# Optimization experiments

Hardware: AMD Instinct MI355X
Metric: run time of the kernel (lower is better)

The kernel has to match this reference:

```python
import jax, jax.numpy as jnp
import numpy as np

H = 1024      # hidden_size
NH = 16       # num_heads
HD = H // NH  # head_dim


def setup_inputs() -> dict:
    key = jax.random.key(0)
    ks = jax.random.split(key, 12)
    inp = {
        "query": jax.random.normal(ks[0], (4, 1024, H), dtype=jnp.float32),
        "key": jax.random.normal(ks[1], (4, 2048, H), dtype=jnp.float32),
        "value": jax.random.normal(ks[2], (4, 2048, H), dtype=jnp.float32),
        "key_padding_mask": jax.random.randint(ks[3], (4, 2048), 0, 2, dtype=jnp.int32),
        # learned parameters (torch Linear: y = x @ W.T + b); we store W already transposed
        "Wq": jax.random.normal(ks[4], (H, H), dtype=jnp.float32) * (1.0 / np.sqrt(H)),
        "bq": jnp.zeros((H,), dtype=jnp.float32),
        "Wk": jax.random.normal(ks[5], (H, H), dtype=jnp.float32) * (1.0 / np.sqrt(H)),
        "bk": jnp.zeros((H,), dtype=jnp.float32),
        "Wv": jax.random.normal(ks[6], (H, H), dtype=jnp.float32) * (1.0 / np.sqrt(H)),
        "bv": jnp.zeros((H,), dtype=jnp.float32),
        "Wo": jax.random.normal(ks[7], (H, H), dtype=jnp.float32) * (1.0 / np.sqrt(H)),
        "bo": jnp.zeros((H,), dtype=jnp.float32),
    }
    return inp


def reference(query, key, value, key_padding_mask, Wq, bq, Wk, bk, Wv, bv, Wo, bo):
    B, Sq, _ = query.shape
    Sk = key.shape[1]
    scaling = HD ** -0.5
    # projections -> [B, NH, S, HD]
    q = (query @ Wq + bq).reshape(B, Sq, NH, HD).transpose(0, 2, 1, 3)
    k = (key @ Wk + bk).reshape(B, Sk, NH, HD).transpose(0, 2, 1, 3)
    v = (value @ Wv + bv).reshape(B, Sk, NH, HD).transpose(0, 2, 1, 3)
    # scores [B, NH, Sq, Sk]
    scores = jnp.einsum("bhqd,bhkd->bhqk", q, k) * scaling
    # mask: positions where key_padding_mask == 0 are ignored
    scores = jnp.where((key_padding_mask == 0)[:, None, None, :], -jnp.inf, scores)
    attn = jax.nn.softmax(scores, axis=-1)
    # dropout is identity in eval mode
    out = jnp.einsum("bhqk,bhkd->bhqd", attn, v)
    out = out.transpose(0, 2, 1, 3).reshape(B, Sq, H)
    return out @ Wo + bo
```

## Files before the change

kernel.cpp:

```cpp
#include <hip/hip_runtime.h>
#include <hip/hip_fp16.h>
#include <math.h>

#define B_ 4
#define SQ 1024
#define SK 2048
#define HH 1024
#define NHEAD 16
#define HDIM 64

typedef _Float16 f16;
typedef __attribute__((ext_vector_type(8))) _Float16 f16x8;
typedef __attribute__((ext_vector_type(4))) _Float16 f16x4;
typedef __attribute__((ext_vector_type(4))) float f32x4;
typedef unsigned int u32;
typedef unsigned long long u64;

#define GLOAD_LDS16(gp, lp) __builtin_amdgcn_global_load_lds( \
    (const __attribute__((address_space(1))) u32*)(gp),        \
    (__attribute__((address_space(3))) u32*)(lp), 16, 0, 0)

__global__ __launch_bounds__(256) void prep_k(
    const float* __restrict__ q, const float* __restrict__ k,
    const float* __restrict__ v,
    const float* __restrict__ W0, const float* __restrict__ W1,
    const float* __restrict__ W2, const float* __restrict__ W3,
    const int* __restrict__ mask,
    f16* __restrict__ qo, f16* __restrict__ ko, f16* __restrict__ vo,
    f16* __restrict__ WT, u32* __restrict__ pmask)
{
    __shared__ f16 t[64 * 80];
    const int bid = blockIdx.x, tid = threadIdx.x;
    if (bid < 10240) {
        int i = bid * 256 + tid;
        const float* src; f16* dst; int j;
        if (i < 524288)       { src = q; dst = qo; j = i; }
        else if (i < 1572864) { src = k; dst = ko; j = i - 524288; }
        else                  { src = v; dst = vo; j = i - 1572864; }
        float4 a = ((const float4*)src)[(size_t)j * 2];
        float4 b = ((const float4*)src)[(size_t)j * 2 + 1];
        f16x8 o;
        o[0] = (f16)a.x; o[1] = (f16)a.y; o[2] = (f16)a.z; o[3] = (f16)a.w;
        o[4] = (f16)b.x; o[5] = (f16)b.y; o[6] = (f16)b.z; o[7] = (f16)b.w;
        *(f16x8*)(dst + (size_t)j * 8) = o;
    } else if (bid < 11264) {
        int id = bid - 10240;
        int z = id >> 8, idx = id & 255;
        const float* W = z == 0 ? W0 : z == 1 ? W1 : z == 2 ? W2 : W3;
        f16* out = WT + (size_t)z * HH * HH;
        const int r0 = (idx >> 4) * 64, c0 = (idx & 15) * 64;
#pragma unroll
        for (int p = 0; p < 4; p++) {
            int s = p * 256 + tid;
            int row = s >> 4, u = s & 15;
            float4 a = *(const float4*)(W + (size_t)(r0 + row) * HH + c0 + u * 4);
            f16x4 vv;
            vv[0] = (f16)a.x; vv[1] = (f16)a.y; vv[2] = (f16)a.z; vv[3] = (f16)a.w;
            *(f16x4*)(t + row * 80 + u * 4) = vv;
        }
        __syncthreads();
#pragma unroll
        for (int p = 0; p < 2; p++) {
            int s = p * 256 + tid;
            int n = s >> 3, u = s & 7;
            f16x8 vv;
#pragma unroll
            for (int j = 0; j < 8; j++) vv[j] = t[(u * 8 + j) * 80 + n];
            *(f16x8*)(out + (size_t)(c0 + n) * HH + r0 + u * 8) = vv;
        }
    } else {
        int j = (bid - 11264) * 256 + tid;
        u64 bal = __ballot(mask[j] != 0);
        if ((tid & 63) == 0) *(u64*)(pmask + ((j >> 6) << 1)) = bal;
    }
}

template <int OUTMODE>
__global__ __launch_bounds__(256) void gemm_k(
    const f16* __restrict__ A, const f16* __restrict__ BT,
    const float* __restrict__ bias, void* __restrict__ Cout,
    int M, int K)
{
    __shared__ f16 sA[2][4096];
    __shared__ f16 sB[2][4096];
    const int tid = threadIdx.x, lane = tid & 63, w = tid >> 6;
    const int nwg = gridDim.x;
    const int swz = ((int)blockIdx.x & 7) * (nwg >> 3) + ((int)blockIdx.x >> 3);
    const int m0 = (swz >> 3) * 128;
    const int n0 = (swz & 7) * 128;
    const int wr = w >> 1, wc = w & 1;
    const int ql = lane & 15, g = lane >> 4;
    const int N = 1024;
    f32x4 acc[4][4] = {};

    auto stage = [&](int buf, int k0) {
#pragma unroll
        for (int p = 0; p < 2; p++) {
            int s = p * 256 + tid;
            int row = s >> 2, us = ((s & 3) ^ (row & 3)) * 8;
            f16* dst = &sA[buf][(p * 256 + w * 64) * 8];
            f16* dstB = &sB[buf][(p * 256 + w * 64) * 8];
            GLOAD_LDS16(A  + (size_t)(m0 + row) * K + k0 + us, dst);
            GLOAD_LDS16(BT + (size_t)(n0 + row) * K + k0 + us, dstB);
        }
    };

    stage(0, 0);
    int cur = 0;
    for (int k0 = 0; k0 < K; k0 += 32) {
        __syncthreads();
        if (k0 + 32 < K) stage(cur ^ 1, k0 + 32);
        f16x8 af[4], bf[4];
#pragma unroll
        for (int m = 0; m < 4; m++) {
            int row = wr * 64 + m * 16 + ql;
            af[m] = *(const f16x8*)(&sA[cur][row * 32 + ((g ^ (row & 3)) * 8)]);
        }
#pragma unroll
        for (int n = 0; n < 4; n++) {
            int row = wc * 64 + n * 16 + ql;
            bf[n] = *(const f16x8*)(&sB[cur][row * 32 + ((g ^ (row & 3)) * 8)]);
        }
#pragma unroll
        for (int m = 0; m < 4; m++)
#pragma unroll
            for (int n = 0; n < 4; n++)
                acc[m][n] = __builtin_amdgcn_mfma_f32_16x16x32_f16(af[m], bf[n], acc[m][n], 0, 0, 0);
        cur ^= 1;
    }

    float bv[4];
#pragma unroll
    for (int n = 0; n < 4; n++) bv[n] = bias[n0 + wc * 64 + n * 16 + ql];
#pragma unroll
    for (int m = 0; m < 4; m++) {
        int row0 = m0 + wr * 64 + m * 16 + g * 4;
#pragma unroll
        for (int n = 0; n < 4; n++) {
            int col = n0 + wc * 64 + n * 16 + ql;
            if (OUTMODE == 2) {
                int bb = row0 >> 11, kk = row0 & 2047;
                int hh = col >> 6, dd = col & 63;
                f16x4 vv;
#pragma unroll
                for (int e = 0; e < 4; e++) vv[e] = (f16)(acc[m][n][e] + bv[n]);
                *(f16x4*)((f16*)Cout + ((size_t)(bb * NHEAD + hh) * HDIM + dd) * SK + kk) = vv;
            } else if (OUTMODE == 1) {
#pragma unroll
                for (int e = 0; e < 4; e++)
                    ((f16*)Cout)[(size_t)(row0 + e) * N + col] = (f16)(acc[m][n][e] + bv[n]);
            } else {
#pragma unroll
                for (int e = 0; e < 4; e++)
                    ((float*)Cout)[(size_t)(row0 + e) * N + col] = acc[m][n][e] + bv[n];
            }
        }
    }
}

#define SC2 0.18033688f
#define THR2 11.5f

__global__ __launch_bounds__(512, 6) void attn_mfma_k(
    const f16* __restrict__ qp,
    const f16* __restrict__ kp,
    const f16* __restrict__ vt,
    const u32* __restrict__ pmask,
    f16* __restrict__ ctx)
{
    const int flat = ((int)blockIdx.x & 7) * 64 + ((int)blockIdx.x >> 3);
    const int qt = flat & 7, h = (flat >> 3) & 15, b = flat >> 7;
    const int q0 = qt * 128;
    const int tid = threadIdx.x, lane = tid & 63, w = tid >> 6;
    const int ql = lane & 15, g = lane >> 4;

    __shared__ f16 ks[2 * 4096];
    __shared__ f16 vs[2 * 4096];
    __shared__ f16 plds[8][16 * 80];
    __shared__ u32 smask[64];

    const f16* kbase = kp + (size_t)b * SK * HH + h * HDIM;
    const f16* vbase = vt + ((size_t)(b * NHEAD + h)) * HDIM * SK;

    if (tid < 64) smask[tid] = pmask[b * 64 + tid];

    f16x8 qf[2];
    {
        const f16* qb = qp + ((size_t)(b * SQ + q0 + w * 16 + ql)) * HH + h * HDIM + g * 8;
        qf[0] = *(const f16x8*)qb;
        qf[1] = *(const f16x8*)(qb + 32);
    }

    auto stageKV = [&](int buf, int kt) {
        int r = tid >> 3, ulg = ((tid & 7) ^ (r & 7)) * 8;
        GLOAD_LDS16(kbase + (size_t)(kt + r) * HH + ulg, ks + buf * 4096 + w * 512);
        GLOAD_LDS16(vbase + (size_t)r * SK + kt + ulg,   vs + buf * 4096 + w * 512);
    };

    f32x4 oacc[4] = {};
    float mrun = -1e30f, lrun = 0.f;

    stageKV(0, 0);
    int cur = 0;
    for (int kt = 0; kt < SK; kt += 64) {
        __syncthreads();
        if (kt + 64 < SK) stageKV(cur ^ 1, kt + 64);
        const f16* kb = ks + cur * 4096;
        const f16* vb = vs + cur * 4096;

        f32x4 sacc[4] = {};
        __builtin_amdgcn_s_setprio(1);
#pragma unroll
        for (int n = 0; n < 4; n++) {
            int key = n * 16 + ql;
#pragma unroll
            for (int df = 0; df < 2; df++) {
                int u = df * 4 + g;
                f16x8 kf = *(const f16x8*)(kb + key * 64 + ((u ^ (key & 7)) * 8));
                sacc[n] = __builtin_amdgcn_mfma_f32_16x16x32_f16(kf, qf[df], sacc[n], 0, 0, 0);
            }
        }
        __builtin_amdgcn_s_setprio(0);

        u32 msh0 = smask[(kt >> 5)]     >> (g * 4);
        u32 msh1 = smask[(kt >> 5) + 1] >> (g * 4);

        float sv[4][4];
        float mt = -1e30f;
#pragma unroll
        for (int n = 0; n < 4; n++) {
            u32 msh = (n < 2) ? msh0 : msh1;
#pragma unroll
            for (int e = 0; e < 4; e++) {
                float bia = ((msh >> (((n & 1) << 4) + e)) & 1u) ? 0.f : -1e30f;
                float s = sacc[n][e] * SC2 + bia;
                sv[n][e] = s;
                mt = fmaxf(mt, s);
            }
        }
        mt = fmaxf(mt, __shfl_xor(mt, 16, 64));
        mt = fmaxf(mt, __shfl_xor(mt, 32, 64));

        if (__any(mt > mrun + THR2)) {
            float mnew = fmaxf(mrun, mt);
            float alpha = __builtin_amdgcn_exp2f(mrun - mnew);
            mrun = mnew;
            lrun *= alpha;
            float al[4];
#pragma unroll
            for (int e = 0; e < 4; e++) al[e] = __shfl(alpha, g * 4 + e, 64);
#pragma unroll
            for (int df = 0; df < 4; df++)
#pragma unroll
                for (int e = 0; e < 4; e++) oacc[df][e] *= al[e];
        }

        float tsum = 0.f;
#pragma unroll
        for (int n = 0; n < 4; n++) {
            float p0 = __builtin_amdgcn_exp2f(sv[n][0] - mrun);
            float p1 = __builtin_amdgcn_exp2f(sv[n][1] - mrun);
            float p2 = __builtin_amdgcn_exp2f(sv[n][2] - mrun);
            float p3 = __builtin_amdgcn_exp2f(sv[n][3] - mrun);
            tsum += (p0 + p1) + (p2 + p3);
            f16x4 pv4;
            pv4[0] = (f16)p0; pv4[1] = (f16)p1; pv4[2] = (f16)p2; pv4[3] = (f16)p3;
            *(f16x4*)(plds[w] + ql * 80 + n * 16 + g * 4) = pv4;
        }
        tsum += __shfl_xor(tsum, 16, 64);
        tsum += __shfl_xor(tsum, 32, 64);
        lrun += tsum;

        __builtin_amdgcn_s_setprio(1);
#pragma unroll
        for (int t = 0; t < 2; t++) {
            f16x8 pf = *(const f16x8*)(plds[w] + ql * 80 + t * 32 + g * 8);
#pragma unroll
            for (int df = 0; df < 4; df++) {
                int d = df * 16 + ql;
                int u = t * 4 + g;
                f16x8 vf = *(const f16x8*)(vb + d * 64 + ((u ^ (d & 7)) * 8));
                oacc[df] = __builtin_amdgcn_mfma_f32_16x16x32_f16(pf, vf, oacc[df], 0, 0, 0);
            }
        }
        __builtin_amdgcn_s_setprio(0);
        cur ^= 1;
    }

    float linv[4];
#pragma unroll
    for (int e = 0; e < 4; e++) {
        float lv = __shfl(lrun, g * 4 + e, 64);
        linv[e] = 1.f / lv;
    }
    f16* ob = ctx + ((size_t)(b * SQ + q0 + w * 16)) * HH + h * HDIM;
#pragma unroll
    for (int df = 0; df < 4; df++)
#pragma unroll
        for (int e = 0; e < 4; e++)
            ob[(size_t)(g * 4 + e) * HH + df * 16 + ql] = (f16)(oacc[df][e] * linv[e]);
}

extern "C" void kernel_launch(void* const* d_in, const int* in_sizes, int n_in,
                              void* d_out, int out_size, void* d_ws, size_t ws_size,
                              hipStream_t stream) {
    const float* query = (const float*)d_in[0];
    const float* key   = (const float*)d_in[1];
    const float* value = (const float*)d_in[2];
    const int*   mask  = (const int*)d_in[3];
    const float* Wq = (const float*)d_in[4];
    const float* bq = (const float*)d_in[5];
    const float* Wk = (const float*)d_in[6];
    const float* bk = (const float*)d_in[7];
    const float* Wv = (const float*)d_in[8];
    const float* bv = (const float*)d_in[9];
    const float* Wo = (const float*)d_in[10];
    const float* bo = (const float*)d_in[11];
    float* out = (float*)d_out;

    const size_t M1 = 1024 * 1024;
    f16* qcast = (f16*)d_ws;
    f16* kcast = qcast + 4 * M1;
    f16* vcast = kcast + 8 * M1;
    f16* wT    = vcast + 8 * M1;
    f16* qp    = wT + 4 * M1;
    f16* kp    = qp + 4 * M1;
    f16* vt    = kp + 8 * M1;
    u32* pmask = (u32*)(vt + 8 * M1);
    f16* ctx   = qcast;

    dim3 blk(256);

    prep_k<<<dim3(11296), blk, 0, stream>>>(query, key, value, Wq, Wk, Wv, Wo,
                                            mask, qcast, kcast, vcast, wT, pmask);

    gemm_k<1><<<dim3(256), blk, 0, stream>>>(qcast, wT + 0 * M1, bq, qp, 4096, HH);
    gemm_k<1><<<dim3(512), blk, 0, stream>>>(kcast, wT + 1 * M1, bk, kp, 8192, HH);
    gemm_k<2><<<dim3(512), blk, 0, stream>>>(vcast, wT + 2 * M1, bv, vt, 8192, HH);

    attn_mfma_k<<<dim3(512), dim3(512), 0, stream>>>(qp, kp, vt, pmask, ctx);

    gemm_k<0><<<dim3(256), blk, 0, stream>>>(ctx, wT + 3 * M1, bo, out, 4096, HH);
}
```

Measured before the change: 192.9 us.

## Fuse QKV projection GEMMs into one launch, shrink Q/O tiles, use float mask bias

```diff
diff --git a/kernel.cpp b/kernel.cpp
--- a/kernel.cpp
+++ b/kernel.cpp
@@ -14,11 +14,13 @@
 typedef __attribute__((ext_vector_type(4))) _Float16 f16x4;
 typedef __attribute__((ext_vector_type(4))) float f32x4;
 typedef unsigned int u32;
-typedef unsigned long long u64;
 
 #define GLOAD_LDS16(gp, lp) __builtin_amdgcn_global_load_lds( \
     (const __attribute__((address_space(1))) u32*)(gp),        \
     (__attribute__((address_space(3))) u32*)(lp), 16, 0, 0)
+#define GLOAD_LDS4(gp, lp) __builtin_amdgcn_global_load_lds(  \
+    (const __attribute__((address_space(1))) u32*)(gp),        \
+    (__attribute__((address_space(3))) u32*)(lp), 4, 0, 0)
 
 __global__ __launch_bounds__(256) void prep_k(
     const float* __restrict__ q, const float* __restrict__ k,
@@ -27,7 +29,7 @@
     const float* __restrict__ W2, const float* __restrict__ W3,
     const int* __restrict__ mask,
     f16* __restrict__ qo, f16* __restrict__ ko, f16* __restrict__ vo,
-    f16* __restrict__ WT, u32* __restrict__ pmask)
+    f16* __restrict__ WT, float* __restrict__ pbias)
 {
     __shared__ f16 t[64 * 80];
     const int bid = blockIdx.x, tid = threadIdx.x;
@@ -70,38 +72,41 @@
         }
     } else {
         int j = (bid - 11264) * 256 + tid;
-        u64 bal = __ballot(mask[j] != 0);
-        if ((tid & 63) == 0) *(u64*)(pmask + ((j >> 6) << 1)) = bal;
-    }
-}
-
-template <int OUTMODE>
-__global__ __launch_bounds__(256) void gemm_k(
+        pbias[j] = mask[j] ? 0.f : -1e30f;
+    }
+}
+
+template <int TM, int OUTMODE>
+__device__ __forceinline__ void gemm_body(
     const f16* __restrict__ A, const f16* __restrict__ BT,
     const float* __restrict__ bias, void* __restrict__ Cout,
-    int M, int K)
-{
-    __shared__ f16 sA[2][4096];
-    __shared__ f16 sB[2][4096];
+    int M, int bid, int nwg, f16* sA, f16* sB)
+{
     const int tid = threadIdx.x, lane = tid & 63, w = tid >> 6;
-    const int nwg = gridDim.x;
-    const int swz = ((int)blockIdx.x & 7) * (nwg >> 3) + ((int)blockIdx.x >> 3);
-    const int m0 = (swz >> 3) * 128;
+    const int swz = (bid & 7) * (nwg >> 3) + (bid >> 3);
+    const int m0 = (swz >> 3) * TM;
     const int n0 = (swz & 7) * 128;
     const int wr = w >> 1, wc = w & 1;
     const int ql = lane & 15, g = lane >> 4;
-    const int N = 1024;
-    f32x4 acc[4][4] = {};
+    const int N = 1024, K = 1024;
+    const int MF = TM / 32;
+    const int ABUF = TM * 32;
+    f32x4 acc[TM / 32][4] = {};
 
     auto stage = [&](int buf, int k0) {
+#pragma unroll
+        for (int p = 0; p < TM / 64; p++) {
+            int s = p * 256 + tid;
+            int row = s >> 2, us = ((s & 3) ^ ((row >> 1) & 3)) * 8;
+            GLOAD_LDS16(A + (size_t)(m0 + row) * K + k0 + us,
+                        sA + buf * ABUF + (p * 256 + w * 64) * 8);
+        }
 #pragma unroll
         for (int p = 0; p < 2; p++) {
             int s = p * 256 + tid;
-            int row = s >> 2, us = ((s & 3) ^ (row & 3)) * 8;
-            f16* dst = &sA[buf][(p * 256 + w * 64) * 8];
-            f16* dstB = &sB[buf][(p * 256 + w * 64) * 8];
-            GLOAD_LDS16(A  + (size_t)(m0 + row) * K + k0 + us, dst);
-            GLOAD_LDS16(BT + (size_t)(n0 + row) * K + k0 + us, dstB);
+            int row = s >> 2, us = ((s & 3) ^ ((row >> 1) & 3)) * 8;
+            GLOAD_LDS16(BT + (size_t)(n0 + row) * K + k0 + us,
+                        sB + buf * 4096 + (p * 256 + w * 64) * 8);
         }
     };
 
@@ -110,19 +115,19 @@
     for (int k0 = 0; k0 < K; k0 += 32) {
         __syncthreads();
         if (k0 + 32 < K) stage(cur ^ 1, k0 + 32);
-        f16x8 af[4], bf[4];
-#pragma unroll
-        for (int m = 0; m < 4; m++) {
-            int row = wr * 64 + m * 16 + ql;
-            af[m] = *(const f16x8*)(&sA[cur][row * 32 + ((g ^ (row & 3)) * 8)]);
+        f16x8 af[MF], bf[4];
+#pragma unroll
+        for (int m = 0; m < MF; m++) {
+            int row = wr * (TM / 2) + m * 16 + ql;
+            af[m] = *(const f16x8*)(sA + cur * ABUF + row * 32 + ((g ^ ((row >> 1) & 3)) * 8));
         }
 #pragma unroll
         for (int n = 0; n < 4; n++) {
             int row = wc * 64 + n * 16 + ql;
-            bf[n] = *(const f16x8*)(&sB[cur][row * 32 + ((g ^ (row & 3)) * 8)]);
-        }
-#pragma unroll
-        for (int m = 0; m < 4; m++)
+            bf[n] = *(const f16x8*)(sB + cur * 4096 + row * 32 + ((g ^ ((row >> 1) & 3)) * 8));
+        }
+#pragma unroll
+        for (int m = 0; m < MF; m++)
 #pragma unroll
             for (int n = 0; n < 4; n++)
                 acc[m][n] = __builtin_amdgcn_mfma_f32_16x16x32_f16(af[m], bf[n], acc[m][n], 0, 0, 0);
@@ -133,8 +138,8 @@
 #pragma unroll
     for (int n = 0; n < 4; n++) bv[n] = bias[n0 + wc * 64 + n * 16 + ql];
 #pragma unroll
-    for (int m = 0; m < 4; m++) {
-        int row0 = m0 + wr * 64 + m * 16 + g * 4;
+    for (int m = 0; m < MF; m++) {
+        int row0 = m0 + wr * (TM / 2) + m * 16 + g * 4;
 #pragma unroll
         for (int n = 0; n < 4; n++) {
             int col = n0 + wc * 64 + n * 16 + ql;
@@ -158,6 +163,34 @@
     }
 }
 
+__global__ __launch_bounds__(256) void qkv_gemm_k(
+    const f16* __restrict__ qc, const f16* __restrict__ kc,
+    const f16* __restrict__ vc, const f16* __restrict__ wT,
+    const float* __restrict__ bq, const float* __restrict__ bk,
+    const float* __restrict__ bv,
+    f16* __restrict__ qp, f16* __restrict__ kp, f16* __restrict__ vt)
+{
+    __shared__ f16 sA[2 * 4096];
+    __shared__ f16 sB[2 * 4096];
+    const int bid = blockIdx.x;
+    const size_t M1 = 1024 * 1024;
+    if (bid < 512)
+        gemm_body<64, 1>(qc, wT, bq, qp, 4096, bid, 512, sA, sB);
+    else if (bid < 1024)
+        gemm_body<128, 1>(kc, wT + M1, bk, kp, 8192, bid - 512, 512, sA, sB);
+    else
+        gemm_body<128, 2>(vc, wT + 2 * M1, bv, vt, 8192, bid - 1024, 512, sA, sB);
+}
+
+__global__ __launch_bounds__(256) void o_gemm_k(
+    const f16* __restrict__ ctx, const f16* __restrict__ wT,
+    const float* __restrict__ bo, float* __restrict__ out)
+{
+    __shared__ f16 sA[2 * 4096];
+    __shared__ f16 sB[2 * 4096];
+    gemm_body<64, 0>(ctx, wT, bo, out, 4096, blockIdx.x, 512, sA, sB);
+}
+
 #define SC2 0.18033688f
 #define THR2 11.5f
 
@@ -165,7 +198,7 @@
     const f16* __restrict__ qp,
     const f16* __restrict__ kp,
     const f16* __restrict__ vt,
-    const u32* __restrict__ pmask,
+    const float* __restrict__ pbias,
     f16* __restrict__ ctx)
 {
     const int flat = ((int)blockIdx.x & 7) * 64 + ((int)blockIdx.x >> 3);
@@ -177,12 +210,11 @@
     __shared__ f16 ks[2 * 4096];
     __shared__ f16 vs[2 * 4096];
     __shared__ f16 plds[8][16 * 80];
-    __shared__ u32 smask[64];
+    __shared__ float sbias[2][64];
 
     const f16* kbase = kp + (size_t)b * SK * HH + h * HDIM;
     const f16* vbase = vt + ((size_t)(b * NHEAD + h)) * HDIM * SK;
-
-    if (tid < 64) smask[tid] = pmask[b * 64 + tid];
+    const float* bbase = pbias + b * SK;
 
     f16x8 qf[2];
     {
@@ -195,6 +227,7 @@
         int r = tid >> 3, ulg = ((tid & 7) ^ (r & 7)) * 8;
         GLOAD_LDS16(kbase + (size_t)(kt + r) * HH + ulg, ks + buf * 4096 + w * 512);
         GLOAD_LDS16(vbase + (size_t)r * SK + kt + ulg,   vs + buf * 4096 + w * 512);
+        if (w == 0) GLOAD_LDS4(bbase + kt + lane, &sbias[buf][0]);
     };
 
     f32x4 oacc[4] = {};
@@ -222,18 +255,15 @@
         }
         __builtin_amdgcn_s_setprio(0);
 
-        u32 msh0 = smask[(kt >> 5)]     >> (g * 4);
-        u32 msh1 = smask[(kt >> 5) + 1] >> (g * 4);
-
         float sv[4][4];
         float mt = -1e30f;
 #pragma unroll
         for (int n = 0; n < 4; n++) {
-            u32 msh = (n < 2) ? msh0 : msh1;
+            float4 b4 = *(const float4*)&sbias[cur][n * 16 + g * 4];
+            float barr[4] = {b4.x, b4.y, b4.z, b4.w};
 #pragma unroll
             for (int e = 0; e < 4; e++) {
-                float bia = ((msh >> (((n & 1) << 4) + e)) & 1u) ? 0.f : -1e30f;
-                float s = sacc[n][e] * SC2 + bia;
+                float s = fmaf(sacc[n][e], SC2, barr[e]);
                 sv[n][e] = s;
                 mt = fmaxf(mt, s);
             }
@@ -326,19 +356,18 @@
     f16* qp    = wT + 4 * M1;
     f16* kp    = qp + 4 * M1;
     f16* vt    = kp + 8 * M1;
-    u32* pmask = (u32*)(vt + 8 * M1);
+    float* pbias = (float*)(vt + 8 * M1);
     f16* ctx   = qcast;
 
     dim3 blk(256);
 
     prep_k<<<dim3(11296), blk, 0, stream>>>(query, key, value, Wq, Wk, Wv, Wo,
-                                            mask, qcast, kcast, vcast, wT, pmask);
-
-    gemm_k<1><<<dim3(256), blk, 0, stream>>>(qcast, wT + 0 * M1, bq, qp, 4096, HH);
-    gemm_k<1><<<dim3(512), blk, 0, stream>>>(kcast, wT + 1 * M1, bk, kp, 8192, HH);
-    gemm_k<2><<<dim3(512), blk, 0, stream>>>(vcast, wT + 2 * M1, bv, vt, 8192, HH);
-
-    attn_mfma_k<<<dim3(512), dim3(512), 0, stream>>>(qp, kp, vt, pmask, ctx);
-
-    gemm_k<0><<<dim3(256), blk, 0, stream>>>(ctx, wT + 3 * M1, bo, out, 4096, HH);
-}
+                                            mask, qcast, kcast, vcast, wT, pbias);
+
+    qkv_gemm_k<<<dim3(1536), blk, 0, stream>>>(qcast, kcast, vcast, wT,
+                                               bq, bk, bv, qp, kp, vt);
+
+    attn_mfma_k<<<dim3(512), dim3(512), 0, stream>>>(qp, kp, vt, pbias, ctx);
+
+    o_gemm_k<<<dim3(512), blk, 0, stream>>>(ctx, wT + 3 * M1, bo, out);
+}
```

Measured after the change: 166.1 us. 1.16x faster.
